# Performance work log

Hardware: AMD Instinct MI355X
Metric: run time of the kernel (lower is better)

Reference implementation:

```python
import jax, jax.numpy as jnp
import numpy as np

EPS = 1e-6
B, T, D = 8, 4096, 512


def setup_inputs() -> dict:
    key = jax.random.key(0)
    ks = jax.random.split(key, 8)
    s = 1.0 / np.sqrt(D)
    return {
        "summarization": jax.random.normal(ks[0], (B, D), jnp.float32),
        "decoder_output": jax.random.normal(ks[1], (B, T, D), jnp.float32),
        "W_hist": jax.random.normal(ks[2], (D, D), jnp.float32) * s,
        "b_hist": jnp.zeros((D,), jnp.float32),
        "W1": jax.random.normal(ks[3], (D, D), jnp.float32) * s,
        "W2": jax.random.normal(ks[4], (D, D), jnp.float32) * s,
        "W_out": jax.random.normal(ks[5], (D, D), jnp.float32) * s,
        "b_out": jnp.zeros((D,), jnp.float32),
        "gamma": jnp.ones((D,), jnp.float32),
        "beta": jnp.zeros((D,), jnp.float32),
    }


def reference(summarization, decoder_output, W_hist, b_hist, W1, W2, W_out, b_out, gamma, beta):
    # Causal running mean: equivalent to tril-mask bmm / row-count, but O(T).
    tgt_len = decoder_output.shape[1]
    counts = jnp.arange(1, tgt_len + 1, dtype=decoder_output.dtype)[None, :, None]
    history = jnp.cumsum(decoder_output, axis=1) / counts            # [B,T,D]
    history = jnp.tanh(history @ W_hist + b_hist)                    # history_linear + tanh
    # TransformMinus: linear1(summ) - linear2(history), then linear_out + tanh
    summ_proj = (summarization @ W1)[:, None, :]                     # [B,1,D] broadcasts over T
    out = summ_proj - history @ W2
    future = jnp.tanh(out @ W_out + b_out)
    # LayerPostprocessing (eval: dropout = identity): LayerNorm(future + decoder_output)
    x = future + decoder_output
    mu = jnp.mean(x, axis=-1, keepdims=True)
    var = jnp.mean(jnp.square(x - mu), axis=-1, keepdims=True)
    return (x - mu) / jnp.sqrt(var + EPS) * gamma + beta
```

## Files before the change

kernel.cpp:

```cpp
#include <hip/hip_runtime.h>
#include <hip/hip_bf16.h>
#include <stdint.h>
#include <stddef.h>

#define DEV static __device__ __forceinline__

typedef __attribute__((ext_vector_type(8))) short short8;
typedef __attribute__((ext_vector_type(4))) float floatx4;

constexpr int Tn = 4096, Dn = 512;
constexpr int NC = 128, CTm = 32;

union U8s { uint4 u4; unsigned short us[8]; };
union U4f { float4 f4; float f[4]; };
union U4s { uint2 u2; unsigned short us[4]; };

DEV float b2f(unsigned short u) {
  union { unsigned int i; float f; } c; c.i = ((unsigned int)u) << 16; return c.f;
}
DEV unsigned short f2b(float f) {
  union { float f; unsigned int u; } c; c.f = f;
  unsigned int r = c.u + 0x7fffu + ((c.u >> 16) & 1u);
  return (unsigned short)(r >> 16);
}
DEV float fast_tanh(float x) {
  float e = __expf(2.0f * x);
  return 1.0f - 2.0f / (e + 1.0f);
}

typedef __attribute__((address_space(1))) void GVOID;
typedef __attribute__((address_space(3))) void LVOID;
DEV void async16(const unsigned short* g, unsigned short* l) {
  __builtin_amdgcn_global_load_lds((GVOID*)g, (LVOID*)l, 16, 0, 0);
}

__global__ void k_fuse1(const float* __restrict__ dec, float* __restrict__ part,
                        const float* __restrict__ Wh, const float* __restrict__ Wo,
                        const float* __restrict__ W1, const float* __restrict__ W2,
                        unsigned short* __restrict__ WhT, unsigned short* __restrict__ WoT,
                        unsigned short* __restrict__ W1b, unsigned short* __restrict__ W2b) {
  int blk = blockIdx.x;
  if (blk < 512) {
    int idx = blk * 256 + threadIdx.x;
    int d4 = idx & 127;
    int c  = (idx >> 7) & (NC - 1);
    int b  = idx >> 14;
    const float* p = dec + ((size_t)b * Tn + (size_t)c * CTm) * Dn + d4 * 4;
    float s[4] = {0,0,0,0};
#pragma unroll 4
    for (int i = 0; i < CTm; ++i) {
      U4f v; v.f4 = *(const float4*)(p + (size_t)i * Dn);
#pragma unroll
      for (int j = 0; j < 4; ++j) s[j] += v.f[j];
    }
    float* o = part + ((size_t)(b * NC + c)) * Dn + d4 * 4;
#pragma unroll
    for (int j = 0; j < 4; ++j) o[j] = s[j];
  } else {
    int wb = blk - 512;
    if (wb < 128) {
      const float* in = (wb < 64) ? Wh : Wo;
      unsigned short* out = (wb < 64) ? WhT : WoT;
      int lb = wb & 63;
      __shared__ float t[64][65];
      int n0 = (lb & 7) * 64, k0 = (lb >> 3) * 64;
#pragma unroll
      for (int l = 0; l < 16; ++l) {
        int lin = l * 256 + threadIdx.x;
        int r = lin >> 6, c = lin & 63;
        t[r][c] = in[(size_t)(k0 + r) * 512 + n0 + c];
      }
      __syncthreads();
#pragma unroll
      for (int l = 0; l < 16; ++l) {
        int lin = l * 256 + threadIdx.x;
        int r = lin >> 6, c = lin & 63;
        out[(size_t)(n0 + r) * 512 + k0 + c] = f2b(t[c][r]);
      }
    } else {
      const float* in = (wb < 160) ? W1 : W2;
      unsigned short* out = (wb < 160) ? W1b : W2b;
      int lb = (wb - 128) & 31;
      size_t base = ((size_t)lb * 256 + threadIdx.x) * 32;
#pragma unroll
      for (int l = 0; l < 8; ++l) {
        U4f v; v.f4 = *(const float4*)(in + base + l * 4);
        U4s o;
#pragma unroll
        for (int j = 0; j < 4; ++j) o.us[j] = f2b(v.f[j]);
        *(uint2*)(out + base + l * 4) = o.u2;
      }
    }
  }
}

template<int EPI>
DEV void gemm256_core(const unsigned short* __restrict__ A, const unsigned short* __restrict__ BT,
                      unsigned short* __restrict__ C, const float* __restrict__ bias,
                      const float* __restrict__ sproj, int m0, int n0) {
  __shared__ alignas(16) unsigned short sA[2][256 * 64];
  __shared__ alignas(16) unsigned short sB[2][256 * 64];
  const int tid  = threadIdx.x;
  const int lane = tid & 63;
  const int w    = tid >> 6;
  const int wr   = w >> 2;
  const int wc   = w & 3;
  const int rs   = lane & 15;
  const int quad = lane >> 4;

  floatx4 acc[8][4];
#pragma unroll
  for (int i = 0; i < 8; ++i)
#pragma unroll
    for (int j = 0; j < 4; ++j) acc[i][j] = (floatx4){0.f, 0.f, 0.f, 0.f};

  auto STAGE = [&](int kt, int buf) {
#pragma unroll
    for (int l = 0; l < 4; ++l) {
      int ch = l * 512 + tid;
      int r  = ch >> 3;
      int kc = ((ch & 7) ^ (r & 7)) * 8;
      async16(A  + (size_t)(m0 + r) * 512 + kt + kc, &sA[buf][ch * 8]);
      async16(BT + (size_t)(n0 + r) * 512 + kt + kc, &sB[buf][ch * 8]);
    }
  };

  auto COMPUTE = [&](int buf) {
    __builtin_amdgcn_s_setprio(1);
#pragma unroll
    for (int kk = 0; kk < 2; ++kk) {
      const int co = ((kk * 4 + quad) ^ (rs & 7)) * 8;
      short8 bfr[4];
#pragma unroll
      for (int nj = 0; nj < 4; ++nj)
        bfr[nj] = *(const short8*)(&sB[buf][(wc * 64 + nj * 16 + rs) * 64 + co]);
#pragma unroll
      for (int mi = 0; mi < 8; ++mi) {
        short8 af = *(const short8*)(&sA[buf][(wr * 128 + mi * 16 + rs) * 64 + co]);
#pragma unroll
        for (int nj = 0; nj < 4; ++nj)
          acc[mi][nj] = __builtin_amdgcn_mfma_f32_16x16x32_bf16(af, bfr[nj], acc[mi][nj], 0, 0, 0);
      }
    }
    __builtin_amdgcn_s_setprio(0);
  };

  STAGE(0, 0);
  for (int t = 0; t < 7; ++t) {
    STAGE((t + 1) * 64, (t + 1) & 1);
    asm volatile("s_waitcnt vmcnt(8)\n\ts_barrier" ::: "memory");
    COMPUTE(t & 1);
    asm volatile("s_barrier" ::: "memory");
  }
  asm volatile("s_waitcnt vmcnt(0)\n\ts_barrier" ::: "memory");
  COMPUTE(1);

#pragma unroll
  for (int mi = 0; mi < 8; ++mi) {
#pragma unroll
    for (int nj = 0; nj < 4; ++nj) {
      const int colg = n0 + wc * 64 + nj * 16 + rs;
#pragma unroll
      for (int r = 0; r < 4; ++r) {
        const int rowg = m0 + wr * 128 + mi * 16 + quad * 4 + r;
        float v = acc[mi][nj][r];
        if constexpr (EPI == 0)      v = fast_tanh(v + bias[colg]);
        else if constexpr (EPI == 3) v = fast_tanh(sproj[(rowg >> 12) * Dn + colg] - v);
        C[(size_t)rowg * 512 + colg] = f2b(v);
      }
    }
  }
}

template<int EPI>
__global__ __launch_bounds__(512, 2)
void k_gemm256(const unsigned short* __restrict__ A, const unsigned short* __restrict__ BT,
               unsigned short* __restrict__ C, const float* __restrict__ bias,
               const float* __restrict__ sproj) {
  gemm256_core<EPI>(A, BT, C, bias, sproj, blockIdx.x * 256, blockIdx.y * 256);
}

__global__ __launch_bounds__(512, 2)
void k_wgemm2(const unsigned short* __restrict__ WoT,
              const unsigned short* __restrict__ W2b, const unsigned short* __restrict__ W1b,
              unsigned short* __restrict__ W2WoT, unsigned short* __restrict__ W1WoT,
              float* __restrict__ part) {
  int blk = blockIdx.x;
  if (blk < 8) {
    const unsigned short* BT = (blk & 4) ? W1b : W2b;
    unsigned short* Cc = (blk & 4) ? W1WoT : W2WoT;
    gemm256_core<2>(WoT, BT, Cc, nullptr, nullptr, (blk & 1) * 256, ((blk >> 1) & 1) * 256);
  } else {
    int idx = (blk - 8) * 512 + threadIdx.x;
    int d4 = idx & 127;
    int b  = idx >> 7;
    float* p = part + (size_t)b * NC * Dn + d4 * 4;
    float s[4] = {0, 0, 0, 0};
    for (int c0 = 0; c0 < NC; c0 += 8) {
      U4f v[8];
#pragma unroll
      for (int i = 0; i < 8; ++i) v[i].f4 = *(const float4*)(p + (size_t)(c0 + i) * Dn);
#pragma unroll
      for (int i = 0; i < 8; ++i) {
        U4f o;
#pragma unroll
        for (int j = 0; j < 4; ++j) { o.f[j] = s[j]; s[j] += v[i].f[j]; }
        *(float4*)(p + (size_t)(c0 + i) * Dn) = o.f4;
      }
    }
  }
}

__global__ void k_fuse3(const float* __restrict__ dec, const float* __restrict__ part,
                        unsigned short* __restrict__ M,
                        const float* __restrict__ summ,
                        const unsigned short* __restrict__ W1WoT,
                        const float* __restrict__ bo, float* __restrict__ spo) {
  int blk = blockIdx.x;
  if (blk < 512) {
    int idx = blk * 256 + threadIdx.x;
    int d4 = idx & 127;
    int c  = (idx >> 7) & (NC - 1);
    int b  = idx >> 14;
    size_t rbase = (size_t)b * Tn + (size_t)c * CTm;
    U4f s; s.f4 = *(const float4*)(part + ((size_t)b * NC + c) * Dn + d4 * 4);
    int t0 = c * CTm;
    const float* dp = dec + rbase * Dn + d4 * 4;
    unsigned short* mp = M + rbase * Dn + d4 * 4;
#pragma unroll 4
    for (int i = 0; i < CTm; ++i) {
      U4f v; v.f4 = *(const float4*)(dp + (size_t)i * Dn);
      float inv = 1.0f / (float)(t0 + i + 1);
      U4s o;
#pragma unroll
      for (int j = 0; j < 4; ++j) { s.f[j] += v.f[j]; o.us[j] = f2b(s.f[j] * inv); }
      *(uint2*)(mp + (size_t)i * Dn) = o.u2;
    }
  } else {
    int widx = (blk - 512) * 4 + (threadIdx.x >> 6);
    int lane = threadIdx.x & 63;
    int n = widx & 511; int b = widx >> 9;
    U8s w8; w8.u4 = *(const uint4*)(W1WoT + (size_t)n * Dn + lane * 8);
    U4f s0, s1;
    s0.f4 = *(const float4*)(summ + (size_t)b * Dn + lane * 8);
    s1.f4 = *(const float4*)(summ + (size_t)b * Dn + lane * 8 + 4);
    float acc = 0.f;
#pragma unroll
    for (int j = 0; j < 4; ++j) acc += s0.f[j] * b2f(w8.us[j]);
#pragma unroll
    for (int j = 0; j < 4; ++j) acc += s1.f[j] * b2f(w8.us[j + 4]);
#pragma unroll
    for (int o = 32; o > 0; o >>= 1) acc += __shfl_xor(acc, o, 64);
    if (lane == 0) spo[(size_t)b * Dn + n] = acc + bo[n];
  }
}

__global__ void k_ln(const unsigned short* __restrict__ F, const float* __restrict__ dec,
                     const float* __restrict__ gamma, const float* __restrict__ beta,
                     float* __restrict__ out) {
  int row  = blockIdx.x * 4 + (threadIdx.x >> 6);
  int lane = threadIdx.x & 63;
  size_t base = (size_t)row * Dn + lane * 8;
  U8s f8; f8.u4 = *(const uint4*)(F + base);
  U4f d0, d1; d0.f4 = *(const float4*)(dec + base); d1.f4 = *(const float4*)(dec + base + 4);
  float x[8]; float s = 0.f, sq = 0.f;
#pragma unroll
  for (int j = 0; j < 8; ++j) {
    float dv = (j < 4) ? d0.f[j] : d1.f[j - 4];
    x[j] = b2f(f8.us[j]) + dv; s += x[j]; sq += x[j] * x[j];
  }
#pragma unroll
  for (int o = 32; o > 0; o >>= 1) { s += __shfl_xor(s, o, 64); sq += __shfl_xor(sq, o, 64); }
  float mu   = s * (1.0f / 512.0f);
  float var  = sq * (1.0f / 512.0f) - mu * mu;
  float rstd = rsqrtf(var + 1e-6f);
  U4f g0, g1, b0, b1, o0, o1;
  g0.f4 = *(const float4*)(gamma + lane * 8); g1.f4 = *(const float4*)(gamma + lane * 8 + 4);
  b0.f4 = *(const float4*)(beta  + lane * 8); b1.f4 = *(const float4*)(beta  + lane * 8 + 4);
#pragma unroll
  for (int j = 0; j < 8; ++j) {
    float g = (j < 4) ? g0.f[j] : g1.f[j - 4];
    float b = (j < 4) ? b0.f[j] : b1.f[j - 4];
    float v = (x[j] - mu) * rstd * g + b;
    if (j < 4) o0.f[j] = v; else o1.f[j - 4] = v;
  }
  *(float4*)(out + base) = o0.f4;
  *(float4*)(out + base + 4) = o1.f4;
}

extern "C" void kernel_launch(void* const* d_in, const int* in_sizes, int n_in,
                              void* d_out, int out_size, void* d_ws, size_t ws_size,
                              hipStream_t stream) {
  (void)in_sizes; (void)n_in; (void)out_size; (void)ws_size;
  const float* summ = (const float*)d_in[0];
  const float* dec  = (const float*)d_in[1];
  const float* Wh   = (const float*)d_in[2];
  const float* bh   = (const float*)d_in[3];
  const float* W1   = (const float*)d_in[4];
  const float* W2   = (const float*)d_in[5];
  const float* Wo   = (const float*)d_in[6];
  const float* bo   = (const float*)d_in[7];
  const float* gam  = (const float*)d_in[8];
  const float* bet  = (const float*)d_in[9];
  float* out = (float*)d_out;

  char* ws = (char*)d_ws;
  unsigned short* Mbuf  = (unsigned short*)(ws);
  unsigned short* Hbuf  = (unsigned short*)(ws + 33554432);
  float*          part  = (float*)(ws + 67108864);
  float*          spo   = (float*)(ws + 69206016);
  unsigned short* WhT   = (unsigned short*)(ws + 69238784);
  unsigned short* WoT   = (unsigned short*)(ws + 69763072);
  unsigned short* W2b   = (unsigned short*)(ws + 70287360);
  unsigned short* W2WoT = (unsigned short*)(ws + 70811648);
  unsigned short* W1b   = (unsigned short*)(ws + 71335936);
  unsigned short* W1WoT = (unsigned short*)(ws + 71860224);

  k_fuse1<<<704, 256, 0, stream>>>(dec, part, Wh, Wo, W1, W2, WhT, WoT, W1b, W2b);

  k_wgemm2<<<10, 512, 0, stream>>>(WoT, W2b, W1b, W2WoT, W1WoT, part);

  k_fuse3<<<1536, 256, 0, stream>>>(dec, part, Mbuf, summ, W1WoT, bo, spo);

  k_gemm256<0><<<dim3(128, 2), 512, 0, stream>>>(Mbuf, WhT, Hbuf, bh, nullptr);
  k_gemm256<3><<<dim3(128, 2), 512, 0, stream>>>(Hbuf, W2WoT, Mbuf, nullptr, spo);

  k_ln<<<8192, 256, 0, stream>>>(Mbuf, dec, gam, bet, out);
}
```

Baseline: 238.5 us.

## Fuse LayerNorm into second GEMM with full-row 128x512 tiles

The GEMM tile changes from 256x256 to 128 rows by the full 512 columns with a K-step of 32, so each block owns complete rows. That lets the second GEMM's epilogue apply tanh, add the residual, and compute the LayerNorm statistics through shuffles and a small shared-memory reduction. The output is then written directly as fp32. This removes the separate LN kernel and the bf16 round-trip of the intermediate, but uses more shared memory for B, more K iterations, and strided scalar epilogue loads and stores of dec and out.

Result: slower. 249.0 us (+4.4%).

```diff
diff --git a/kernel.cpp b/kernel.cpp
--- a/kernel.cpp
+++ b/kernel.cpp
@@ -95,11 +95,20 @@
 }
 
 template<int EPI>
-DEV void gemm256_core(const unsigned short* __restrict__ A, const unsigned short* __restrict__ BT,
-                      unsigned short* __restrict__ C, const float* __restrict__ bias,
-                      const float* __restrict__ sproj, int m0, int n0) {
-  __shared__ alignas(16) unsigned short sA[2][256 * 64];
-  __shared__ alignas(16) unsigned short sB[2][256 * 64];
+DEV void gemm_core(const unsigned short* __restrict__ A,
+                   const unsigned short* __restrict__ BT,
+                   unsigned short* __restrict__ C,
+                   const float* __restrict__ bias,
+                   const float* __restrict__ spo,
+                   const float* __restrict__ dec,
+                   const float* __restrict__ gamma,
+                   const float* __restrict__ beta,
+                   float* __restrict__ out,
+                   int m0) {
+  __shared__ alignas(16) unsigned short sA[2][128 * 32];
+  __shared__ alignas(16) unsigned short sB[2][512 * 32];
+  __shared__ float lnS[128][4];
+  __shared__ float lnQ[128][4];
   const int tid  = threadIdx.x;
   const int lane = tid & 63;
   const int w    = tid >> 6;
@@ -108,76 +117,135 @@
   const int rs   = lane & 15;
   const int quad = lane >> 4;
 
-  floatx4 acc[8][4];
-#pragma unroll
-  for (int i = 0; i < 8; ++i)
-#pragma unroll
-    for (int j = 0; j < 4; ++j) acc[i][j] = (floatx4){0.f, 0.f, 0.f, 0.f};
+  floatx4 acc[4][8];
+#pragma unroll
+  for (int i = 0; i < 4; ++i)
+#pragma unroll
+    for (int j = 0; j < 8; ++j) acc[i][j] = (floatx4){0.f, 0.f, 0.f, 0.f};
 
   auto STAGE = [&](int kt, int buf) {
+    {
+      int r = tid >> 2, c = tid & 3;
+      int kc = (c ^ (r & 3)) * 8;
+      async16(A + (size_t)(m0 + r) * 512 + kt + kc, &sA[buf][tid * 8]);
+    }
 #pragma unroll
     for (int l = 0; l < 4; ++l) {
       int ch = l * 512 + tid;
-      int r  = ch >> 3;
-      int kc = ((ch & 7) ^ (r & 7)) * 8;
-      async16(A  + (size_t)(m0 + r) * 512 + kt + kc, &sA[buf][ch * 8]);
-      async16(BT + (size_t)(n0 + r) * 512 + kt + kc, &sB[buf][ch * 8]);
+      int r = ch >> 2, c = ch & 3;
+      int kc = (c ^ (r & 3)) * 8;
+      async16(BT + (size_t)r * 512 + kt + kc, &sB[buf][ch * 8]);
     }
   };
 
   auto COMPUTE = [&](int buf) {
     __builtin_amdgcn_s_setprio(1);
-#pragma unroll
-    for (int kk = 0; kk < 2; ++kk) {
-      const int co = ((kk * 4 + quad) ^ (rs & 7)) * 8;
-      short8 bfr[4];
-#pragma unroll
-      for (int nj = 0; nj < 4; ++nj)
-        bfr[nj] = *(const short8*)(&sB[buf][(wc * 64 + nj * 16 + rs) * 64 + co]);
-#pragma unroll
-      for (int mi = 0; mi < 8; ++mi) {
-        short8 af = *(const short8*)(&sA[buf][(wr * 128 + mi * 16 + rs) * 64 + co]);
-#pragma unroll
-        for (int nj = 0; nj < 4; ++nj)
-          acc[mi][nj] = __builtin_amdgcn_mfma_f32_16x16x32_bf16(af, bfr[nj], acc[mi][nj], 0, 0, 0);
-      }
+    const int co = (quad ^ (rs & 3)) * 8;
+    short8 bfr[8];
+#pragma unroll
+    for (int nj = 0; nj < 8; ++nj)
+      bfr[nj] = *(const short8*)(&sB[buf][(wc * 128 + nj * 16 + rs) * 32 + co]);
+#pragma unroll
+    for (int mi = 0; mi < 4; ++mi) {
+      short8 af = *(const short8*)(&sA[buf][(wr * 64 + mi * 16 + rs) * 32 + co]);
+#pragma unroll
+      for (int nj = 0; nj < 8; ++nj)
+        acc[mi][nj] = __builtin_amdgcn_mfma_f32_16x16x32_bf16(af, bfr[nj], acc[mi][nj], 0, 0, 0);
     }
     __builtin_amdgcn_s_setprio(0);
   };
 
   STAGE(0, 0);
-  for (int t = 0; t < 7; ++t) {
-    STAGE((t + 1) * 64, (t + 1) & 1);
-    asm volatile("s_waitcnt vmcnt(8)\n\ts_barrier" ::: "memory");
+  for (int t = 0; t < 15; ++t) {
+    STAGE((t + 1) * 32, (t + 1) & 1);
+    asm volatile("s_waitcnt vmcnt(5)\n\ts_barrier" ::: "memory");
     COMPUTE(t & 1);
     asm volatile("s_barrier" ::: "memory");
   }
   asm volatile("s_waitcnt vmcnt(0)\n\ts_barrier" ::: "memory");
   COMPUTE(1);
 
-#pragma unroll
-  for (int mi = 0; mi < 8; ++mi) {
-#pragma unroll
-    for (int nj = 0; nj < 4; ++nj) {
-      const int colg = n0 + wc * 64 + nj * 16 + rs;
+  if constexpr (EPI == 0 || EPI == 2) {
+#pragma unroll
+    for (int nj = 0; nj < 8; ++nj) {
+      const int colg = wc * 128 + nj * 16 + rs;
+      float bb = (EPI == 0) ? bias[colg] : 0.f;
+#pragma unroll
+      for (int mi = 0; mi < 4; ++mi) {
+#pragma unroll
+        for (int r = 0; r < 4; ++r) {
+          const int rowg = m0 + wr * 64 + mi * 16 + quad * 4 + r;
+          float v = acc[mi][nj][r];
+          if constexpr (EPI == 0) v = fast_tanh(v + bb);
+          C[(size_t)rowg * 512 + colg] = f2b(v);
+        }
+      }
+    }
+  } else {
+    const int bidx = m0 >> 12;
+    float spv[8], gv[8], bv[8];
+    int colv[8];
+#pragma unroll
+    for (int nj = 0; nj < 8; ++nj) {
+      colv[nj] = wc * 128 + nj * 16 + rs;
+      spv[nj] = spo[bidx * Dn + colv[nj]];
+      gv[nj]  = gamma[colv[nj]];
+      bv[nj]  = beta[colv[nj]];
+    }
+#pragma unroll
+    for (int mi = 0; mi < 4; ++mi) {
 #pragma unroll
       for (int r = 0; r < 4; ++r) {
-        const int rowg = m0 + wr * 128 + mi * 16 + quad * 4 + r;
-        float v = acc[mi][nj][r];
-        if constexpr (EPI == 0)      v = fast_tanh(v + bias[colg]);
-        else if constexpr (EPI == 3) v = fast_tanh(sproj[(rowg >> 12) * Dn + colg] - v);
-        C[(size_t)rowg * 512 + colg] = f2b(v);
-      }
-    }
-  }
-}
-
-template<int EPI>
+        const int lrow = wr * 64 + mi * 16 + quad * 4 + r;
+        const size_t rowg = (size_t)(m0 + lrow);
+        float s = 0.f, sq = 0.f;
+#pragma unroll
+        for (int nj = 0; nj < 8; ++nj) {
+          float dv = dec[rowg * 512 + colv[nj]];
+          float xf = fast_tanh(spv[nj] - acc[mi][nj][r]) + dv;
+          acc[mi][nj][r] = xf;
+          s += xf; sq += xf * xf;
+        }
+#pragma unroll
+        for (int o = 8; o > 0; o >>= 1) { s += __shfl_xor(s, o, 64); sq += __shfl_xor(sq, o, 64); }
+        if (rs == 0) { lnS[lrow][wc] = s; lnQ[lrow][wc] = sq; }
+      }
+    }
+    __syncthreads();
+#pragma unroll
+    for (int mi = 0; mi < 4; ++mi) {
+#pragma unroll
+      for (int r = 0; r < 4; ++r) {
+        const int lrow = wr * 64 + mi * 16 + quad * 4 + r;
+        const size_t rowg = (size_t)(m0 + lrow);
+        float s = 0.f, sq = 0.f;
+#pragma unroll
+        for (int k = 0; k < 4; ++k) { s += lnS[lrow][k]; sq += lnQ[lrow][k]; }
+        float mu   = s * (1.0f / 512.0f);
+        float var  = sq * (1.0f / 512.0f) - mu * mu;
+        float rstd = rsqrtf(var + 1e-6f);
+#pragma unroll
+        for (int nj = 0; nj < 8; ++nj)
+          out[rowg * 512 + colv[nj]] = (acc[mi][nj][r] - mu) * rstd * gv[nj] + bv[nj];
+      }
+    }
+  }
+}
+
 __global__ __launch_bounds__(512, 2)
-void k_gemm256(const unsigned short* __restrict__ A, const unsigned short* __restrict__ BT,
-               unsigned short* __restrict__ C, const float* __restrict__ bias,
-               const float* __restrict__ sproj) {
-  gemm256_core<EPI>(A, BT, C, bias, sproj, blockIdx.x * 256, blockIdx.y * 256);
+void k_gemmH(const unsigned short* __restrict__ A, const unsigned short* __restrict__ BT,
+             unsigned short* __restrict__ C, const float* __restrict__ bias) {
+  gemm_core<0>(A, BT, C, bias, nullptr, nullptr, nullptr, nullptr, nullptr,
+               blockIdx.x * 128);
+}
+
+__global__ __launch_bounds__(512, 2)
+void k_gemmFLN(const unsigned short* __restrict__ A, const unsigned short* __restrict__ BT,
+               const float* __restrict__ spo, const float* __restrict__ dec,
+               const float* __restrict__ gamma, const float* __restrict__ beta,
+               float* __restrict__ out) {
+  gemm_core<5>(A, BT, nullptr, nullptr, spo, dec, gamma, beta, out,
+               blockIdx.x * 128);
 }
 
 __global__ __launch_bounds__(512, 2)
@@ -189,7 +257,8 @@
   if (blk < 8) {
     const unsigned short* BT = (blk & 4) ? W1b : W2b;
     unsigned short* Cc = (blk & 4) ? W1WoT : W2WoT;
-    gemm256_core<2>(WoT, BT, Cc, nullptr, nullptr, (blk & 1) * 256, ((blk >> 1) & 1) * 256);
+    gemm_core<2>(WoT, BT, Cc, nullptr, nullptr, nullptr, nullptr, nullptr, nullptr,
+                 (blk & 3) * 128);
   } else {
     int idx = (blk - 8) * 512 + threadIdx.x;
     int d4 = idx & 127;
@@ -255,39 +324,6 @@
   }
 }
 
-__global__ void k_ln(const unsigned short* __restrict__ F, const float* __restrict__ dec,
-                     const float* __restrict__ gamma, const float* __restrict__ beta,
-                     float* __restrict__ out) {
-  int row  = blockIdx.x * 4 + (threadIdx.x >> 6);
-  int lane = threadIdx.x & 63;
-  size_t base = (size_t)row * Dn + lane * 8;
-  U8s f8; f8.u4 = *(const uint4*)(F + base);
-  U4f d0, d1; d0.f4 = *(const float4*)(dec + base); d1.f4 = *(const float4*)(dec + base + 4);
-  float x[8]; float s = 0.f, sq = 0.f;
-#pragma unroll
-  for (int j = 0; j < 8; ++j) {
-    float dv = (j < 4) ? d0.f[j] : d1.f[j - 4];
-    x[j] = b2f(f8.us[j]) + dv; s += x[j]; sq += x[j] * x[j];
-  }
-#pragma unroll
-  for (int o = 32; o > 0; o >>= 1) { s += __shfl_xor(s, o, 64); sq += __shfl_xor(sq, o, 64); }
-  float mu   = s * (1.0f / 512.0f);
-  float var  = sq * (1.0f / 512.0f) - mu * mu;
-  float rstd = rsqrtf(var + 1e-6f);
-  U4f g0, g1, b0, b1, o0, o1;
-  g0.f4 = *(const float4*)(gamma + lane * 8); g1.f4 = *(const float4*)(gamma + lane * 8 + 4);
-  b0.f4 = *(const float4*)(beta  + lane * 8); b1.f4 = *(const float4*)(beta  + lane * 8 + 4);
-#pragma unroll
-  for (int j = 0; j < 8; ++j) {
-    float g = (j < 4) ? g0.f[j] : g1.f[j - 4];
-    float b = (j < 4) ? b0.f[j] : b1.f[j - 4];
-    float v = (x[j] - mu) * rstd * g + b;
-    if (j < 4) o0.f[j] = v; else o1.f[j - 4] = v;
-  }
-  *(float4*)(out + base) = o0.f4;
-  *(float4*)(out + base + 4) = o1.f4;
-}
-
 extern "C" void kernel_launch(void* const* d_in, const int* in_sizes, int n_in,
                               void* d_out, int out_size, void* d_ws, size_t ws_size,
                               hipStream_t stream) {
@@ -322,8 +358,7 @@
 
   k_fuse3<<<1536, 256, 0, stream>>>(dec, part, Mbuf, summ, W1WoT, bo, spo);
 
-  k_gemm256<0><<<dim3(128, 2), 512, 0, stream>>>(Mbuf, WhT, Hbuf, bh, nullptr);
-  k_gemm256<3><<<dim3(128, 2), 512, 0, stream>>>(Hbuf, W2WoT, Mbuf, nullptr, spo);
-
-  k_ln<<<8192, 256, 0, stream>>>(Mbuf, dec, gam, bet, out);
-}
+  k_gemmH<<<256, 512, 0, stream>>>(Mbuf, WhT, Hbuf, bh);
+
+  k_gemmFLN<<<256, 512, 0, stream>>>(Hbuf, W2WoT, spo, dec, gam, bet, out);
+}
```
